# Optimization experiments

Measured on AMD Instinct MI355X. Metric: run time of the kernel, lower is better.

Reference implementation:

```python
import jax, jax.numpy as jnp
import numpy as np

T, NC, NQ = 16, 32, 32
H, W, C = 128, 128, 1
DW, DR, DZ = 256, 256, 128
LABEL_DIM, Y_DIM = 2, 2
NHEADS = 8
NFEAT = int(DW * np.log(DW))  # performer default nb_features = int(d*ln d) = 1419


def setup_inputs() -> dict:
    key = jax.random.key(0)
    ks = iter(jax.random.split(key, 48))
    def nrm(shape, scale=0.02):
        return jax.random.normal(next(ks), shape, dtype=jnp.float32) * scale
    z = lambda *s: jnp.zeros(s, jnp.float32)
    return {
        'batch_train_images': jax.random.normal(next(ks), (T, NC, C, H, W), jnp.float32),
        'label_train': jax.random.normal(next(ks), (T, NC, LABEL_DIM), jnp.float32),
        'batch_test_images': jax.random.normal(next(ks), (T, NQ, C, H, W), jnp.float32),
        'conv1_w': nrm((32, C, 3, 3), 0.1), 'conv1_b': z(32),
        'conv2_w': nrm((48, 32, 3, 3), 0.05), 'conv2_b': z(48),
        'conv3_w': nrm((64, 48, 3, 3), 0.05), 'conv3_b': z(64),
        'enc_lw': nrm((DW, 4096)), 'enc_lb': z(DW),
        'ty_w': nrm((DW // 4, LABEL_DIM)), 'ty_b': z(DW // 4),
        'er_w1': nrm((DR, DW + DW // 4), 0.05), 'er_b1': z(DR),
        'er_w2': nrm((DR, DR), 0.05), 'er_b2': z(DR),
        'er_w3': nrm((DR, DR), 0.05), 'er_b3': z(DR),
        'wq': nrm((NHEADS, DW, DW), 0.05), 'wq_b': z(NHEADS, DW),
        'wk': nrm((NHEADS, DW, DW), 0.05), 'wk_b': z(NHEADS, DW),
        'wv': nrm((NHEADS, DW, DW), 0.05), 'wv_b': z(NHEADS, DW),
        'wo_w': nrm((DW, NHEADS * DW), 0.02), 'wo_b': z(DW),
        'rz_w': nrm((DZ, DR), 0.05), 'rz_b': z(DZ),
        'd0_w1': nrm((100, DW + DZ), 0.05), 'd0_b1': z(100),
        'd0_w2': nrm((100, 100), 0.05), 'd0_b2': z(100),
        'd0_w3': nrm((Y_DIM, 100), 0.05), 'd0_b3': z(Y_DIM),
        'proj': jax.random.normal(next(ks), (NFEAT, DW), jnp.float32),
    }


def _conv(x, w, b, stride):
    y = jax.lax.conv_general_dilated(x, w, (stride, stride), [(1, 1), (1, 1)],
                                     dimension_numbers=('NCHW', 'OIHW', 'NCHW'))
    return y + b[None, :, None, None]


def _maxpool2(x):
    return jax.lax.reduce_window(x, -jnp.inf, jax.lax.max, (1, 1, 2, 2), (1, 1, 2, 2), 'VALID')


def _encode(x, c1w, c1b, c2w, c2b, c3w, c3b, lw, lb):
    # BBBEncoder (mean weights): 128->64->32->pool16->8, 64ch, flatten 4096 -> DW
    x = jax.nn.relu(_conv(x, c1w, c1b, 2))
    x = jax.nn.relu(_conv(x, c2w, c2b, 2))
    x = _maxpool2(x)
    x = jax.nn.relu(_conv(x, c3w, c3b, 2))
    x = x.reshape(x.shape[0], -1)  # [B, 4096], NCHW order matches torch view
    return x @ lw.T + lb


def _softmax_kernel(x, proj, is_query):
    # performer softmax-kernel random features
    dn = x.shape[-1] ** -0.25
    ratio = proj.shape[0] ** -0.5
    xn = x * dn
    xd = jnp.einsum('bhnd,fd->bhnf', xn, proj)
    diag = 0.5 * jnp.sum(xn * xn, axis=-1, keepdims=True)
    if is_query:
        m = jnp.max(xd, axis=-1, keepdims=True)
    else:
        m = jnp.max(xd, axis=(-1, -2), keepdims=True)
    return ratio * (jnp.exp(xd - diag - jax.lax.stop_gradient(m)) + 1e-4)


def _forward(batch_train_images, label_train, batch_test_images,
             conv1_w, conv1_b, conv2_w, conv2_b, conv3_w, conv3_b, enc_lw, enc_lb,
             ty_w, ty_b, er_w1, er_b1, er_w2, er_b2, er_w3, er_b3,
             wq, wq_b, wk, wk_b, wv, wv_b, wo_w, wo_b, rz_w, rz_b,
             d0_w1, d0_b1, d0_w2, d0_b2, d0_w3, d0_b3, proj):
    enc = lambda im: _encode(im, conv1_w, conv1_b, conv2_w, conv2_b, conv3_w, conv3_b, enc_lw, enc_lb)
    x_qry = enc(batch_test_images.reshape(-1, C, H, W)).reshape(T, NQ, DW)
    x_ctx = enc(batch_train_images.reshape(-1, C, H, W)).reshape(T, NC, DW)
    ly = label_train @ ty_w.T + ty_b
    x = jnp.concatenate([x_ctx, ly], axis=2)  # [T, NC, DW + DW//4]
    h = jax.nn.relu(x @ er_w1.T + er_b1)
    h = jax.nn.relu(h @ er_w2.T + er_b2)
    rs = h @ er_w3.T + er_b3  # [T, NC, DR]
    # per-head projections (batched over the 8 heads)
    k_all = jnp.einsum('bnd,hed->bhne', x_ctx, wk) + wk_b[None, :, None, :]
    v_all = jnp.einsum('bnd,hed->bhne', rs, wv) + wv_b[None, :, None, :]
    q_all = jnp.einsum('bnd,hed->bhne', x_qry, wq) + wq_b[None, :, None, :]
    qp = _softmax_kernel(q_all, proj, True)   # [T, H, NQ, F]
    kp = _softmax_kernel(k_all, proj, False)  # [T, H, NC, F]
    d_inv = 1.0 / jnp.einsum('bhnf,bhf->bhn', qp, kp.sum(axis=2))
    ctx_mat = jnp.einsum('bhnf,bhne->bhfe', kp, v_all)
    outs = jnp.einsum('bhnf,bhfe->bhne', qp, ctx_mat) * d_inv[..., None]
    outs = outs.transpose(0, 2, 3, 1).reshape(T, NQ, -1)  # permute(0,2,3,1).view
    rep = outs @ wo_w.T + wo_b
    zz = rep @ rz_w.T + rz_b  # [T, NQ, DZ]
    xz = jnp.concatenate([x_qry, zz], axis=-1)
    h = jax.nn.relu(xz @ d0_w1.T + d0_b1)
    h = jax.nn.relu(h @ d0_w2.T + d0_b2)
    return jnp.tanh(h @ d0_w3.T + d0_b3)  # pr_y_mu [T, NQ, Y_DIM]


def reference(batch_train_images, label_train, batch_test_images,
              conv1_w, conv1_b, conv2_w, conv2_b, conv3_w, conv3_b, enc_lw, enc_lb,
              ty_w, ty_b, er_w1, er_b1, er_w2, er_b2, er_w3, er_b3,
              wq, wq_b, wk, wk_b, wv, wv_b, wo_w, wo_b, rz_w, rz_b,
              d0_w1, d0_b1, d0_w2, d0_b2, d0_w3, d0_b3, proj):
    pr_y_mu = _forward(batch_train_images, label_train, batch_test_images,
                       conv1_w, conv1_b, conv2_w, conv2_b, conv3_w, conv3_b, enc_lw, enc_lb,
                       ty_w, ty_b, er_w1, er_b1, er_w2, er_b2, er_w3, er_b3,
                       wq, wq_b, wk, wk_b, wv, wv_b, wo_w, wo_b, rz_w, rz_b,
                       d0_w1, d0_b1, d0_w2, d0_b2, d0_w3, d0_b3, proj)
    kl = jnp.float32(0.0)  # deterministic (mean-weight) BBB encoder -> KL constant
    return (pr_y_mu, kl)
```

## Files before the change

### kernel.cpp

```cpp
#include <hip/hip_runtime.h>
#include <math.h>

#define F_FEAT 1419
static constexpr float DN    = 0.25f;

typedef short short8 __attribute__((ext_vector_type(8)));
typedef float f32x4  __attribute__((ext_vector_type(4)));

static constexpr long OFF_XDQ  = 0;
static constexpr long OFF_XDK  = 5812224;
static constexpr long U_WQH = 0;
static constexpr long U_WQL = 524288;
static constexpr long U_WKH = 1048576;
static constexpr long U_WKL = 1572864;
static constexpr long U_WVH = 2097152;
static constexpr long U_WVL = 2621440;
static constexpr long OFF_ENCT = 4000000;
static constexpr long OFF_REPT = 6200000;
static constexpr long OFF_PA   = 11624448;
static constexpr long U_PH  = 23248896;
static constexpr long U_PL  = 23625728;
static constexpr long U_XCH = 24002560;
static constexpr long U_XCL = 24264704;
static constexpr long U_RSH = 24526848;
static constexpr long U_RSL = 24657920;
static constexpr long U_C3H = 25165824;
static constexpr long U_C3L = 29360128;
static constexpr long U_WOH = 25165824;
static constexpr long U_WOL = 25690112;
static constexpr long BASE     = 16777216;
static constexpr long OFF_XCTX = BASE + 0;
static constexpr long OFF_XQRY = BASE + 131072;
static constexpr long OFF_XCAT = BASE + 262144;
static constexpr long OFF_H1   = BASE + 425984;
static constexpr long OFF_H2   = BASE + 557056;
static constexpr long OFF_RS   = BASE + 688128;
static constexpr long U_QH  = (BASE + 819200) * 2;
static constexpr long U_QL  = U_QH + 1048576;
static constexpr long U_KH  = (BASE + 1867776) * 2;
static constexpr long U_KL  = U_KH + 1048576;
static constexpr long OFF_VA   = BASE + 2916352;
static constexpr long OFF_AW1  = BASE + 3964928;
static constexpr long U_ELH = (BASE + 3977344) * 2;
static constexpr long U_ELL = U_ELH + 1048576;
static constexpr long U_REPH = U_ELH;
static constexpr long U_REPL = U_ELL;
static constexpr long OFF_REP  = BASE + 5025920;
static constexpr long OFF_XZ   = BASE + 5156992;
static constexpr long OFF_DH1  = BASE + 5353600;
static constexpr long OFF_DH2  = BASE + 5404800;
static constexpr long OFF_MD   = BASE + 5456000;
static constexpr long OFF_AW   = 22233216;
static constexpr long OFF_AW3  = 22240128;

__device__ inline unsigned short f2bf(float f) {
    unsigned int x = __float_as_uint(f);
    unsigned int r = x + 0x7fffu + ((x >> 16) & 1u);
    return (unsigned short)(r >> 16);
}
__device__ inline float bf2f(unsigned short h) {
    return __uint_as_float((unsigned int)h << 16);
}
__device__ inline unsigned int cvtpk(float a, float b) {
    unsigned int r;
    asm("v_cvt_pk_bf16_f32 %0, %1, %2" : "=v"(r) : "v"(a), "v"(b));
    return r;
}

static constexpr int NA1 = 13824;
static constexpr int NA2 = NA1 + 1024;
static constexpr int NA3 = NA2 + 73728;
static constexpr int NA4 = NA3 + 1048576;

__global__ void k_wprepA(const float* __restrict__ w2, const float* __restrict__ w1,
                         const float* __restrict__ w3, const float* __restrict__ elw,
                         unsigned short* __restrict__ Aw, unsigned short* __restrict__ Aw1,
                         unsigned short* __restrict__ Aw3,
                         unsigned short* __restrict__ ELh, unsigned short* __restrict__ ELl)
{
    int i = blockIdx.x * 256 + threadIdx.x;
    if (i < NA1) {
        int ic  = i & 31;
        int m16 = (i >> 5) & 15;
        int emt = i >> 9;
        int mt  = emt % 3, e = emt / 3;
        Aw[i] = f2bf(w2[((mt * 16 + m16) * 32 + ic) * 9 + e]);
    } else if (i < NA2) {
        int j = i - NA1;
        int k = j & 31, m = (j >> 5) & 15, mt = j >> 9;
        Aw1[j] = (k < 9) ? f2bf(w1[(mt * 16 + m) * 9 + k]) : (unsigned short)0;
    } else if (i < NA3) {
        int j = i - NA2;
        int k  = j & 63;
        int m  = (j >> 6) & 15;
        int hl = (j >> 10) & 1;
        int mt = (j >> 11) & 3;
        int e  = j >> 13;
        unsigned short v = 0;
        if (k < 48) {
            float w = w3[((mt * 16 + m) * 48 + k) * 9 + e];
            unsigned short hi = f2bf(w);
            v = hl == 0 ? hi : f2bf(w - bf2f(hi));
        }
        Aw3[j] = v;
    } else if (i < NA4) {
        int j = i - NA3;
        float v = elw[j];
        unsigned short h = f2bf(v);
        ELh[j] = h; ELl[j] = f2bf(v - bf2f(h));
    }
}

static constexpr int NB1 = 376832;
static constexpr int NB2 = NB1 + 1572864;

__global__ void k_wprepB(const float* __restrict__ proj,
                         const float* __restrict__ wq, const float* __restrict__ wk,
                         const float* __restrict__ wv,
                         unsigned short* __restrict__ Ph, unsigned short* __restrict__ Pl,
                         unsigned short* __restrict__ Wqkv)
{
    int i = blockIdx.x * 256 + threadIdx.x;
    if (i < NB1) {
        float v = (i < 363264) ? proj[i] : 0.f;
        unsigned short h = f2bf(v);
        Ph[i] = h; Pl[i] = f2bf(v - bf2f(h));
    } else if (i < NB2) {
        int j = i - NB1;
        int y = j / 524288, jj = j % 524288;
        const float* s = (y == 0) ? wq : (y == 1) ? wk : wv;
        float v = s[jj];
        unsigned short h = f2bf(v);
        Wqkv[(long)y * 1048576 + jj] = h;
        Wqkv[(long)y * 1048576 + 524288 + jj] = f2bf(v - bf2f(h));
    }
}

#define TP 136
__launch_bounds__(256)
__global__ void k_conv12m(const float* __restrict__ train, const float* __restrict__ test,
                          const float* __restrict__ b1,
                          const unsigned short* __restrict__ Aw,
                          const unsigned short* __restrict__ Aw1,
                          const float* __restrict__ b2,
                          unsigned short* __restrict__ pool_out)
{
    const int g   = blockIdx.x;
    const int img = blockIdx.y;
    const float* in = (img < 512) ? (train + (long)img * 16384)
                                  : (test  + (long)(img - 512) * 16384);

    __shared__ unsigned short ring[9 * 66 * 40];
    __shared__ unsigned short tile[19 * TP];

    const int t = threadIdx.x;

    for (int i = t; i < 9 * 40; i += 256) {
        int sl = i / 40, icp = i % 40;
        ring[(sl * 66 + 0) * 40 + icp] = 0;
    }
    if (g == 0)
        for (int i = t; i < 66 * 40; i += 256) ring[i] = 0;
    if (t < 19) *(unsigned int*)&tile[t * TP + 2] = 0u;

    {
        const float4 z4 = make_float4(0.f, 0.f, 0.f, 0.f);
        for (int u = t; u < 19 * 32; u += 256) {
            int row = u >> 5, k = u & 31;
            int r2 = 16 * g - 3 + row;
            float4 v = (r2 >= 0) ? *(const float4*)(in + r2 * 128 + k * 4) : z4;
            uint2 d;
            d.x = cvtpk(v.x, v.y);
            d.y = cvtpk(v.z, v.w);
            *(uint2*)&tile[row * TP + 4 + k * 4] = d;
        }
    }
    __syncthreads();

    const int w    = t >> 6;
    const int lane = t & 63;
    const int cn   = lane & 15;
    const int quad = lane >> 4;

    short8 a1f0 = *(const short8*)&Aw1[(0 * 16 + cn) * 32 + quad * 8];
    short8 a1f1 = *(const short8*)&Aw1[(16 + cn) * 32 + quad * 8];
    float4 bsa = *(const float4*)&b1[quad * 4];
    float4 bsb = *(const float4*)&b1[16 + quad * 4];

    const int px2 = w * 16 + cn;
    const int tb  = 2 * px2 + 2;
    auto do_slice = [&](int sl) {
        const int rb = 2 * sl * TP + tb;
        uint4 pk = make_uint4(0u, 0u, 0u, 0u);
        if (quad == 0) {
            unsigned int w00 = *(const unsigned int*)&tile[rb];
            unsigned int w10 = *(const unsigned int*)&tile[rb + 2];
            unsigned int w01 = *(const unsigned int*)&tile[rb + TP];
            unsigned int w11 = *(const unsigned int*)&tile[rb + TP + 2];
            unsigned int w02 = *(const unsigned int*)&tile[rb + 2 * TP];
            unsigned int w12 = *(const unsigned int*)&tile[rb + 2 * TP + 2];
            pk.x = (w00 >> 16) | (w10 << 16);
            pk.y = (w10 >> 16) | (w01 & 0xffff0000u);
            pk.z = w11;
            pk.w = (w02 >> 16) | (w12 << 16);
        } else if (quad == 1) {
            pk.x = (*(const unsigned int*)&tile[rb + 2 * TP + 2]) >> 16;
        }
        short8 bfr = *(const short8*)&pk;
        f32x4 z = (f32x4){0.f, 0.f, 0.f, 0.f};
        f32x4 c0 = __builtin_amdgcn_mfma_f32_16x16x32_bf16(a1f0, bfr, z, 0, 0, 0);
        f32x4 c1 = __builtin_amdgcn_mfma_f32_16x16x32_bf16(a1f1, bfr, z, 0, 0, 0);
        uint2 u0, u1;
        u0.x = cvtpk(fmaxf(c0[0] + bsa.x, 0.f), fmaxf(c0[1] + bsa.y, 0.f));
        u0.y = cvtpk(fmaxf(c0[2] + bsa.z, 0.f), fmaxf(c0[3] + bsa.w, 0.f));
        u1.x = cvtpk(fmaxf(c1[0] + bsb.x, 0.f), fmaxf(c1[1] + bsb.y, 0.f));
        u1.y = cvtpk(fmaxf(c1[2] + bsb.z, 0.f), fmaxf(c1[3] + bsb.w, 0.f));
        *(uint2*)&ring[(sl * 66 + px2 + 1) * 40 + quad * 4]      = u0;
        *(uint2*)&ring[(sl * 66 + px2 + 1) * 40 + 16 + quad * 4] = u1;
    };
    if (g > 0) do_slice(0);
    #pragma unroll
    for (int sl = 1; sl < 9; sl++) do_slice(sl);

    short8 ca0 = *(const short8*)&Aw[((0 * 3 + 0) * 16 + cn) * 32 + quad * 8];
    short8 ca1 = *(const short8*)&Aw[((0 * 3 + 1) * 16 + cn) * 32 + quad * 8];
    short8 ca2 = *(const short8*)&Aw[((0 * 3 + 2) * 16 + cn) * 32 + quad * 8];
    __syncthreads();

    const int pr = w >> 1, xh = w & 1;
    f32x4 acc[3][2];
    #pragma unroll
    for (int mt = 0; mt < 3; mt++) {
        acc[mt][0] = (f32x4){0.f, 0.f, 0.f, 0.f};
        acc[mt][1] = (f32x4){0.f, 0.f, 0.f, 0.f};
    }

    #pragma unroll
    for (int e = 0; e < 9; e++) {
        int dy = e / 3, dx = e - 3 * dy;
        int c  = 2 * (xh * 16 + cn) + dx;
        int s0 = 4 * pr + dy;
        short8 b0  = *(const short8*)&ring[(s0 * 66 + c) * 40 + quad * 8];
        short8 b1f = *(const short8*)&ring[((s0 + 2) * 66 + c) * 40 + quad * 8];
        short8 na0, na1, na2;
        if (e < 8) {
            na0 = *(const short8*)&Aw[(((e + 1) * 3 + 0) * 16 + cn) * 32 + quad * 8];
            na1 = *(const short8*)&Aw[(((e + 1) * 3 + 1) * 16 + cn) * 32 + quad * 8];
            na2 = *(const short8*)&Aw[(((e + 1) * 3 + 2) * 16 + cn) * 32 + quad * 8];
        }
        acc[0][0] = __builtin_amdgcn_mfma_f32_16x16x32_bf16(ca0, b0,  acc[0][0], 0, 0, 0);
        acc[1][0] = __builtin_amdgcn_mfma_f32_16x16x32_bf16(ca1, b0,  acc[1][0], 0, 0, 0);
        acc[2][0] = __builtin_amdgcn_mfma_f32_16x16x32_bf16(ca2, b0,  acc[2][0], 0, 0, 0);
        acc[0][1] = __builtin_amdgcn_mfma_f32_16x16x32_bf16(ca0, b1f, acc[0][1], 0, 0, 0);
        acc[1][1] = __builtin_amdgcn_mfma_f32_16x16x32_bf16(ca1, b1f, acc[1][1], 0, 0, 0);
        acc[2][1] = __builtin_amdgcn_mfma_f32_16x16x32_bf16(ca2, b1f, acc[2][1], 0, 0, 0);
        if (e < 8) { ca0 = na0; ca1 = na1; ca2 = na2; }
    }

    {
        const int prow = 2 * g + pr;
        const int ppx  = xh * 8 + (cn >> 1);
        unsigned short* pb = pool_out + ((long)img * 256 + prow * 16 + ppx) * 96
                           + ((cn & 1) ? 48 : 0);
        #pragma unroll
        for (int mt = 0; mt < 3; mt++) {
            float4 bv = *(const float4*)&b2[mt * 16 + quad * 4];
            float m0, m1, m2, m3;
            {
                float v;
                v = fmaxf(fmaxf(acc[mt][0][0] + bv.x, acc[mt][1][0] + bv.x), 0.f);
                m0 = fmaxf(v, __shfl_xor(v, 1));
                v = fmaxf(fmaxf(acc[mt][0][1] + bv.y, acc[mt][1][1] + bv.y), 0.f);
                m1 = fmaxf(v, __shfl_xor(v, 1));
                v = fmaxf(fmaxf(acc[mt][0][2] + bv.z, acc[mt][1][2] + bv.z), 0.f);
                m2 = fmaxf(v, __shfl_xor(v, 1));
                v = fmaxf(fmaxf(acc[mt][0][3] + bv.w, acc[mt][1][3] + bv.w), 0.f);
                m3 = fmaxf(v, __shfl_xor(v, 1));
            }
            uint2 hv;
            hv.x = cvtpk(m0, m1);
            hv.y = cvtpk(m2, m3);
            uint2 sv = hv;
            if (cn & 1) {
                float d0 = m0 - bf2f((unsigned short)(hv.x & 0xffffu));
                float d1 = m1 - bf2f((unsigned short)(hv.x >> 16));
                float d2 = m2 - bf2f((unsigned short)(hv.y & 0xffffu));
                float d3 = m3 - bf2f((unsigned short)(hv.y >> 16));
                sv.x = cvtpk(d0, d1);
                sv.y = cvtpk(d2, d3);
            }
            *(uint2*)&pb[mt * 16 + quad * 4] = sv;
        }
    }
}

#define C3PITCH 104
__launch_bounds__(512)
__global__ void k_conv3m(const unsigned short* __restrict__ pool,
                         const unsigned short* __restrict__ Aw3,
                         const float* __restrict__ b3,
                         unsigned short* __restrict__ C3h, unsigned short* __restrict__ C3l)
{
    const int img = blockIdx.x;
    __shared__ unsigned short s_in[30120];
    const int t = threadIdx.x;

    uint4* s4 = (uint4*)s_in;
    const uint4 zz = make_uint4(0, 0, 0, 0);
    for (int i = t; i < 3765; i += 512) s4[i] = zz;
    __syncthreads();
    {
        int p = t >> 1, half = t & 1;
        const uint4* src = (const uint4*)(pool + ((long)img * 256 + p) * 96 + half * 48);
        int r = p >> 4, c = p & 15;
        uint4* dst = (uint4*)(s_in + ((r + 1) * 17 + (c + 1)) * C3PITCH + half * 48);
        #pragma unroll
        for (int j = 0; j < 6; j++) dst[j] = src[j];
    }
    __syncthreads();

    const int w = t >> 6, lane = t & 63;
    const int n = lane & 15, quad = lane >> 4;
    const int mt = w >> 1, ntb = (w & 1) * 2;

    f32x4 acc[2];
    acc[0] = (f32x4){0.f, 0.f, 0.f, 0.f};
    acc[1] = (f32x4){0.f, 0.f, 0.f, 0.f};

    for (int e = 0; e < 9; e++) {
        int dy = e / 3, dx = e - 3 * dy;
        const unsigned short* A0 = Aw3 + (long)(((e * 4 + mt) * 2 + 0) * 16 + n) * 64 + quad * 8;
        const unsigned short* A1 = Aw3 + (long)(((e * 4 + mt) * 2 + 1) * 16 + n) * 64 + quad * 8;
        short8 ah0 = *(const short8*)(A0);
        short8 ah1 = *(const short8*)(A0 + 32);
        short8 al0 = *(const short8*)(A1);
        short8 al1 = *(const short8*)(A1 + 32);
        #pragma unroll
        for (int j = 0; j < 2; j++) {
            int p = (ntb + j) * 16 + n;
            int y = p >> 3, x = p & 7;
            const unsigned short* Bp = s_in + ((2 * y + dy) * 17 + (2 * x + dx)) * C3PITCH + quad * 8;
            short8 bh0 = *(const short8*)(Bp);
            short8 bh1 = *(const short8*)(Bp + 32);
            short8 bl0 = *(const short8*)(Bp + 48);
            short8 bl1 = *(const short8*)(Bp + 48 + 32);
            acc[j] = __builtin_amdgcn_mfma_f32_16x16x32_bf16(ah0, bh0, acc[j], 0, 0, 0);
            acc[j] = __builtin_amdgcn_mfma_f32_16x16x32_bf16(ah1, bh1, acc[j], 0, 0, 0);
            acc[j] = __builtin_amdgcn_mfma_f32_16x16x32_bf16(ah0, bl0, acc[j], 0, 0, 0);
            acc[j] = __builtin_amdgcn_mfma_f32_16x16x32_bf16(ah1, bl1, acc[j], 0, 0, 0);
            acc[j] = __builtin_amdgcn_mfma_f32_16x16x32_bf16(al0, bh0, acc[j], 0, 0, 0);
            acc[j] = __builtin_amdgcn_mfma_f32_16x16x32_bf16(al1, bh1, acc[j], 0, 0, 0);
        }
    }

    unsigned short* oh = C3h + (long)img * 4096;
    unsigned short* ol = C3l + (long)img * 4096;
    #pragma unroll
    for (int reg = 0; reg < 4; reg++) {
        int oc = mt * 16 + quad * 4 + reg;
        float bias = b3[oc];
        #pragma unroll
        for (int j = 0; j < 2; j++) {
            int p = (ntb + j) * 16 + n;
            float v = fmaxf(acc[j][reg] + bias, 0.f);
            unsigned short h = f2bf(v);
            oh[oc * 64 + p] = h;
            ol[oc * 64 + p] = f2bf(v - bf2f(h));
        }
    }
}

template<int OUTMODE>
__launch_bounds__(256)
__global__ void mgemm(const unsigned short* __restrict__ Xh0, const unsigned short* __restrict__ Xl0,
                      const unsigned short* __restrict__ Wph, const unsigned short* __restrict__ Wpl,
                      const float* __restrict__ Bb, float* __restrict__ Yf,
                      unsigned short* __restrict__ Yh, unsigned short* __restrict__ Yl,
                      int M, int N, int K, int ldY, float scale,
                      long sX, long sW, long sB, long sY, int kChunk)
{
    const int z = blockIdx.z;
    const unsigned short* Xh = Xh0 + (OUTMODE == 3 ? 0 : (long)z * sX);
    const unsigned short* Xl = Xl0 + (OUTMODE == 3 ? 0 : (long)z * sX);
    const unsigned short* Wh = Wph + (OUTMODE == 3 ? 0 : (long)z * sW);
    const unsigned short* Wl = Wpl + (OUTMODE == 3 ? 0 : (long)z * sW);
    const float* B = Bb ? (Bb + (OUTMODE == 3 ? 0 : (long)z * sB)) : nullptr;
    int k0 = 0, k1 = K;
    if (OUTMODE == 3) { k0 = z * kChunk; k1 = min(K, k0 + kChunk); }

    __shared__ unsigned short sAh[64 * 40], sAl[64 * 40], sBh[64 * 40], sBl[64 * 40];

    const int t = threadIdx.x;
    const int m0 = blockIdx.y * 64, n0 = blockIdx.x * 64;
    const int r = t >> 2, kq = (t & 3) * 8;

    const int w = t >> 6, lane = t & 63;
    const int wm = (w & 1) * 32, wn = (w >> 1) * 32;
    const int cn = lane & 15, quad = lane >> 4;

    f32x4 acc[2][2];
    acc[0][0] = acc[0][1] = acc[1][0] = acc[1][1] = (f32x4){0.f, 0.f, 0.f, 0.f};

    for (int kb = k0; kb < k1; kb += 32) {
        *(uint4*)&sAh[r * 40 + kq] = *(const uint4*)&Xh[(long)(m0 + r) * K + kb + kq];
        *(uint4*)&sAl[r * 40 + kq] = *(const uint4*)&Xl[(long)(m0 + r) * K + kb + kq];
        *(uint4*)&sBh[r * 40 + kq] = *(const uint4*)&Wh[(long)(n0 + r) * K + kb + kq];
        *(uint4*)&sBl[r * 40 + kq] = *(const uint4*)&Wl[(long)(n0 + r) * K + kb + kq];
        __syncthreads();
        short8 axh[2], axl[2], bxh[2], bxl[2];
        #pragma unroll
        for (int i = 0; i < 2; i++) {
            axh[i] = *(const short8*)&sAh[(wm + i * 16 + cn) * 40 + quad * 8];
            axl[i] = *(const short8*)&sAl[(wm + i * 16 + cn) * 40 + quad * 8];
            bxh[i] = *(const short8*)&sBh[(wn + i * 16 + cn) * 40 + quad * 8];
            bxl[i] = *(const short8*)&sBl[(wn + i * 16 + cn) * 40 + quad * 8];
        }
        #pragma unroll
        for (int i = 0; i < 2; i++)
            #pragma unroll
            for (int j = 0; j < 2; j++) {
                acc[i][j] = __builtin_amdgcn_mfma_f32_16x16x32_bf16(axh[i], bxh[j], acc[i][j], 0, 0, 0);
                acc[i][j] = __builtin_amdgcn_mfma_f32_16x16x32_bf16(axh[i], bxl[j], acc[i][j], 0, 0, 0);
                acc[i][j] = __builtin_amdgcn_mfma_f32_16x16x32_bf16(axl[i], bxh[j], acc[i][j], 0, 0, 0);
            }
        __syncthreads();
    }

    #pragma unroll
    for (int i = 0; i < 2; i++) {
        #pragma unroll
        for (int reg = 0; reg < 4; reg++) {
            int row = m0 + wm + i * 16 + quad * 4 + reg;
            #pragma unroll
            for (int j = 0; j < 2; j++) {
                int col = n0 + wn + j * 16 + cn;
                if (col >= N) continue;
                float v = acc[i][j][reg] * scale;
                if (OUTMODE == 3) {
                    (Yf + (long)z * sY)[(long)row * ldY + col] = v;
                } else if (OUTMODE == 0) {
                    if (B) v += B[col];
                    (Yf + (long)z * sY)[(long)row * ldY + col] = v;
                } else {
                    if (B) v += B[col];
                    unsigned short h = f2bf(v);
                    (Yh + (long)z * sY)[(long)row * ldY + col] = h;
                    (Yl + (long)z * sY)[(long)row * ldY + col] = f2bf(v - bf2f(h));
                }
            }
        }
    }
}

__global__ void k_red_enc(const float* __restrict__ tmp, const float* __restrict__ elb,
                          float* __restrict__ x_ctx, unsigned short* __restrict__ XCh,
                          unsigned short* __restrict__ XCl, float* __restrict__ xcat,
                          const float* __restrict__ label, const float* __restrict__ tyw,
                          const float* __restrict__ tyb,
                          const float* __restrict__ wow, unsigned short* __restrict__ WOh,
                          unsigned short* __restrict__ WOl)
{
    int b = blockIdx.x;
    int tt = threadIdx.x;
    if (b < 1024) {
        int i = b * 256 + tt;
        int r = i >> 8, c = i & 255;
        float v = elb[c];
        #pragma unroll
        for (int z = 0; z < 8; z++) v += tmp[(long)z * 262144 + i];
        x_ctx[i] = v;
        unsigned short h = f2bf(v);
        XCh[i] = h; XCl[i] = f2bf(v - bf2f(h));
        if (r < 512) xcat[r * 320 + c] = v;
    } else if (b < 1152) {
        int i = (b - 1024) * 256 + tt;
        int r = i >> 6, e = i & 63;
        xcat[r * 320 + 256 + e] = tyb[e] + label[r * 2] * tyw[e * 2] + label[r * 2 + 1] * tyw[e * 2 + 1];
    } else {
        int i = (b - 1152) * 256 + tt;
        float v = wow[i];
        unsigned short h = f2bf(v);
        WOh[i] = h; WOl[i] = f2bf(v - bf2f(h));
    }
}

__global__ void k_red_rep(const float* __restrict__ tmp, const float* __restrict__ wob,
                          float* __restrict__ rep,
                          const float* __restrict__ xq, float* __restrict__ xz)
{
    int b = blockIdx.x;
    int tt = threadIdx.x;
    if (b < 512) {
        int i = b * 256 + tt;
        int c = i & 255;
        float v = wob[c];
        #pragma unroll
        for (int z = 0; z < 4; z++) v += tmp[(long)z * 131072 + i];
        rep[i] = v;
    } else {
        int i = (b - 512) * 256 + tt;
        int r = i >> 8, c = i & 255;
        xz[r * 384 + c] = xq[i];
    }
}

template<int BM, int BN, int BK, int ACT, bool FIN, bool WP>
__launch_bounds__(256)
__global__ void gemm_k(const float* __restrict__ X, const float* __restrict__ W,
                       const float* __restrict__ B, float* __restrict__ Y,
                       int M, int N, int K, int ldY,
                       unsigned short* __restrict__ Ph2, unsigned short* __restrict__ Pl2)
{
    __shared__ float As[BK][BM + 4];
    __shared__ float Bs[BK][BN + 4];
    const int t = threadIdx.x;
    const int tx = t & 15, ty = t >> 4;
    const int m0 = blockIdx.y * BM, n0 = blockIdx.x * BN;
    float acc[2][2] = {{0.f, 0.f}, {0.f, 0.f}};

    for (int kb = 0; kb < K; kb += BK) {
        for (int i = t; i < BM * BK; i += 256) {
            int rr = i / BK, c = i % BK;
            int mm = m0 + rr, kk = kb + c;
            As[c][rr] = (mm < M && kk < K) ? X[(long)mm * K + kk] : 0.f;
        }
        for (int i = t; i < BN * BK; i += 256) {
            int rr = i / BK, c = i % BK;
            int nn = n0 + rr, kk = kb + c;
            Bs[c][rr] = (nn < N && kk < K) ? W[(long)nn * K + kk] : 0.f;
        }
        __syncthreads();
        #pragma unroll
        for (int kk = 0; kk < BK; kk++) {
            float2 a2 = *(const float2*)&As[kk][ty * 2];
            float2 b2 = *(const float2*)&Bs[kk][tx * 2];
            acc[0][0] += a2.x * b2.x; acc[0][1] += a2.x * b2.y;
            acc[1][0] += a2.y * b2.x; acc[1][1] += a2.y * b2.y;
        }
        __syncthreads();
    }

    #pragma unroll
    for (int i = 0; i < 2; i++) {
        int mm = m0 + ty * 2 + i;
        if (mm >= M) continue;
        #pragma unroll
        for (int j = 0; j < 2; j++) {
            int nn = n0 + tx * 2 + j;
            if (nn >= N) continue;
            float v = acc[i][j] + (B ? B[nn] : 0.f);
            if (ACT == 1) v = fmaxf(v, 0.f);
            if (ACT == 2) v = tanhf(v);
            Y[(long)mm * ldY + nn] = v;
            if (WP) {
                unsigned short h = f2bf(v);
                Ph2[(long)mm * ldY + nn] = h;
                Pl2[(long)mm * ldY + nn] = f2bf(v - bf2f(h));
            }
        }
    }
    if (FIN && t == 0 && blockIdx.x == 0 && blockIdx.y == 0) Y[1024] = 0.f;
}

__launch_bounds__(256)
__global__ void k_maxdiag(const float* __restrict__ xdq, const float* __restrict__ xdk,
                          const unsigned short* __restrict__ Qh, const unsigned short* __restrict__ Ql,
                          const unsigned short* __restrict__ Kh, const unsigned short* __restrict__ Kl,
                          float* __restrict__ dq, float* __restrict__ mq,
                          float* __restrict__ dk, float* __restrict__ mk)
{
    __shared__ float red[8];
    const int bx = blockIdx.x;
    const int t = threadIdx.x;

    if (bx < 4096) {
        const int tok = bx;
        float v = bf2f(Qh[(long)tok * 256 + t]) + bf2f(Ql[(long)tok * 256 + t]);
        float s = v * v;
        for (int d = 1; d < 64; d <<= 1) s += __shfl_xor(s, d);
        if ((t & 63) == 0) red[t >> 6] = s;

        float m = -1e30f;
        #pragma unroll
        for (int j = 0; j < 6; j++) {
            int f = t + j * 256;
            if (f < F_FEAT) m = fmaxf(m, xdq[(long)tok * F_FEAT + f]);
        }
        for (int d = 1; d < 64; d <<= 1) m = fmaxf(m, __shfl_xor(m, d));
        if ((t & 63) == 0) red[4 + (t >> 6)] = m;
        __syncthreads();
        if (t == 0) {
            dq[tok] = (red[0] + red[1] + red[2] + red[3]) * (1.f / 32.f);
            mq[tok] = fmaxf(fmaxf(red[4], red[5]), fmaxf(red[6], red[7]));
        }
    } else {
        const int kb = bx - 4096;
        const long tok0 = (long)kb * 32;
        const int row = t >> 3, j = t & 7;

        float s = 0.f;
        const unsigned short* ph = Kh + (tok0 + row) * 256 + j * 32;
        const unsigned short* pl = Kl + (tok0 + row) * 256 + j * 32;
        for (int q = 0; q < 32; q++) { float v = bf2f(ph[q]) + bf2f(pl[q]); s += v * v; }
        s += __shfl_xor(s, 1); s += __shfl_xor(s, 2); s += __shfl_xor(s, 4);
        if (j == 0) dk[tok0 + row] = s * (1.f / 32.f);

        const float* base = xdk + tok0 * F_FEAT;
        float m = -1e30f;
        for (int i = t; i < 32 * F_FEAT; i += 256) m = fmaxf(m, base[i]);
        for (int d = 1; d < 64; d <<= 1) m = fmaxf(m, __shfl_xor(m, d));
        if ((t & 63) == 0) red[t >> 6] = m;
        __syncthreads();
        if (t == 0) mk[kb] = fmaxf(fmaxf(red[0], red[1]), fmaxf(red[2], red[3]));
    }
}

#define NSPLIT 4
#define FCH 355
__launch_bounds__(256)
__global__ void k_attn1(const float* __restrict__ qp, const float* __restrict__ kp,
                        const float* __restrict__ dq, const float* __restrict__ mq,
                        const float* __restrict__ dk, const float* __restrict__ mk,
                        float* __restrict__ pA)
{
    const int s  = blockIdx.x;
    const int kb = blockIdx.y;
    const long row0 = (long)kb * 32;
    const int f0 = s * FCH;
    const int f1 = min(F_FEAT, f0 + FCH);

    __shared__ float s_q[32 * 65];
    __shared__ float s_k[32 * 65];
    __shared__ float s_cq[32], s_ck[32];

    const int t = threadIdx.x;
    const int n = t >> 3;
    const int mq_ = (t & 7) * 4;

    if (t < 32) {
        s_cq[t] = dq[row0 + t] + mq[row0 + t];
        s_ck[t] = dk[row0 + t] + mk[kb];
    }
    __syncthreads();

    float acc[4] = {0.f, 0.f, 0.f, 0.f};
    for (int fc = f0; fc < f1; fc += 64) {
        for (int i = t; i < 2048; i += 256) {
            int rr = i >> 6, ff = i & 63;
            int fg = fc + ff;
            float qv = 0.f, kv = 0.f;
            if (fg < f1) {
                qv = expf(qp[(row0 + rr) * F_FEAT + fg] - s_cq[rr]) + 1e-4f;
                kv = expf(kp[(row0 + rr) * F_FEAT + fg] - s_ck[rr]) + 1e-4f;
            }
            s_q[rr * 65 + ff] = qv;
            s_k[rr * 65 + ff] = kv;
        }
        __syncthreads();
        #pragma unroll 8
        for (int ff = 0; ff < 64; ff++) {
            float a = s_q[n * 65 + ff];
            #pragma unroll
            for (int j = 0; j < 4; j++) acc[j] += a * s_k[(mq_ + j) * 65 + ff];
        }
        __syncthreads();
    }

    float* dst = pA + ((long)kb * NSPLIT + s) * 1024;
    #pragma unroll
    for (int j = 0; j < 4; j++) dst[n * 32 + mq_ + j] = acc[j];
}

__launch_bounds__(256)
__global__ void k_attn2(const float* __restrict__ pA, const float* __restrict__ va,
                        unsigned short* __restrict__ REPh, unsigned short* __restrict__ REPl)
{
    const int ec = blockIdx.x;
    const int kb = blockIdx.y;
    const int h = kb >> 4, tt = kb & 15;
    const long row0 = (long)kb * 32;

    __shared__ float s_A[32][33];
    __shared__ float s_di[32];
    __shared__ float s_v[32 * 64];

    const int t = threadIdx.x;

    {
        const float* base = pA + (long)kb * NSPLIT * 1024 + t * 4;
        float4 v0 = *(const float4*)(base);
        float4 v1 = *(const float4*)(base + 1024);
        float4 v2 = *(const float4*)(base + 2048);
        float4 v3 = *(const float4*)(base + 3072);
        int r = t >> 3, c = (t & 7) * 4;
        s_A[r][c]     = v0.x + v1.x + v2.x + v3.x;
        s_A[r][c + 1] = v0.y + v1.y + v2.y + v3.y;
        s_A[r][c + 2] = v0.z + v1.z + v2.z + v3.z;
        s_A[r][c + 3] = v0.w + v1.w + v2.w + v3.w;
    }
    for (int i = t; i < 2048; i += 256) {
        int m = i >> 6, e = i & 63;
        s_v[m * 64 + e] = va[row0 * 256 + m * 256 + ec * 64 + e];
    }
    __syncthreads();
    if (t < 32) {
        float s = 0.f;
        #pragma unroll
        for (int m = 0; m < 32; m++) s += s_A[t][m];
        s_di[t] = 1.f / s;
    }
    __syncthreads();

    const int n = t >> 3, e0 = t & 7;
    float out[8];
    #pragma unroll
    for (int j = 0; j < 8; j++) out[j] = 0.f;
    for (int m = 0; m < 32; m++) {
        float a = s_A[n][m];
        #pragma unroll
        for (int j = 0; j < 8; j++) out[j] += a * s_v[m * 64 + e0 + 8 * j];
    }
    float di = s_di[n];
    unsigned short* dsth = REPh + ((long)tt * 32 + n) * 2048;
    unsigned short* dstl = REPl + ((long)tt * 32 + n) * 2048;
    #pragma unroll
    for (int j = 0; j < 8; j++) {
        int e = ec * 64 + e0 + 8 * j;
        float val = out[j] * di;
        unsigned short hh = f2bf(val);
        dsth[e * 8 + h] = hh;
        dstl[e * 8 + h] = f2bf(val - bf2f(hh));
    }
}

extern "C" void kernel_launch(void* const* d_in, const int* in_sizes, int n_in,
                              void* d_out, int out_size, void* d_ws, size_t ws_size,
                              hipStream_t stream)
{
    const float* train  = (const float*)d_in[0];
    const float* label  = (const float*)d_in[1];
    const float* test   = (const float*)d_in[2];
    const float* c1w = (const float*)d_in[3];  const float* c1b = (const float*)d_in[4];
    const float* c2w = (const float*)d_in[5];  const float* c2b = (const float*)d_in[6];
    const float* c3w = (const float*)d_in[7];  const float* c3b = (const float*)d_in[8];
    const float* elw = (const float*)d_in[9];  const float* elb = (const float*)d_in[10];
    const float* tyw = (const float*)d_in[11]; const float* tyb = (const float*)d_in[12];
    const float* ew1 = (const float*)d_in[13]; const float* eb1 = (const float*)d_in[14];
    const float* ew2 = (const float*)d_in[15]; const float* eb2 = (const float*)d_in[16];
    const float* ew3 = (const float*)d_in[17]; const float* eb3 = (const float*)d_in[18];
    const float* wq  = (const float*)d_in[19]; const float* wqb = (const float*)d_in[20];
    const float* wk  = (const float*)d_in[21]; const float* wkb = (const float*)d_in[22];
    const float* wv  = (const float*)d_in[23]; const float* wvb = (const float*)d_in[24];
    const float* wow = (const float*)d_in[25]; const float* wob = (const float*)d_in[26];
    const float* rzw = (const float*)d_in[27]; const float* rzb = (const float*)d_in[28];
    const float* dw1 = (const float*)d_in[29]; const float* db1 = (const float*)d_in[30];
    const float* dw2 = (const float*)d_in[31]; const float* db2 = (const float*)d_in[32];
    const float* dw3 = (const float*)d_in[33]; const float* db3 = (const float*)d_in[34];
    const float* proj= (const float*)d_in[35];

    float* wsf = (float*)d_ws;
    unsigned short* usw = (unsigned short*)d_ws;
    float* out = (float*)d_out;

    unsigned short* A_pool = usw;
    float* x_ctx  = wsf + OFF_XCTX;
    float* x_qry  = wsf + OFF_XQRY;
    float* xcat   = wsf + OFF_XCAT;
    float* h1     = wsf + OFF_H1;
    float* h2     = wsf + OFF_H2;
    float* rs     = wsf + OFF_RS;
    float* v_all  = wsf + OFF_VA;
    float* rep    = wsf + OFF_REP;
    float* xz     = wsf + OFF_XZ;
    float* dh1    = wsf + OFF_DH1;
    float* dh2    = wsf + OFF_DH2;
    float* xd_q   = wsf + OFF_XDQ;
    float* xd_k   = wsf + OFF_XDK;
    float* enc_t  = wsf + OFF_ENCT;
    float* rep_t  = wsf + OFF_REPT;
    float* pA     = wsf + OFF_PA;
    float* dqv    = wsf + OFF_MD;
    float* mqv    = wsf + OFF_MD + 4096;
    float* dkv    = wsf + OFF_MD + 8192;
    float* mkv    = wsf + OFF_MD + 12288;
    unsigned short* Aw  = (unsigned short*)(wsf + OFF_AW);
    unsigned short* Aw3 = (unsigned short*)(wsf + OFF_AW3);
    unsigned short* Aw1 = (unsigned short*)(wsf + OFF_AW1);

    unsigned short* Wqkv = usw + U_WQH;
    unsigned short* WQh = usw + U_WQH; unsigned short* WQl = usw + U_WQL;
    unsigned short* WKh = usw + U_WKH; unsigned short* WKl = usw + U_WKL;
    unsigned short* WVh = usw + U_WVH; unsigned short* WVl = usw + U_WVL;
    unsigned short* Ph  = usw + U_PH;  unsigned short* Pl  = usw + U_PL;
    unsigned short* XCh = usw + U_XCH; unsigned short* XCl = usw + U_XCL;
    unsigned short* RSh = usw + U_RSH; unsigned short* RSl = usw + U_RSL;
    unsigned short* C3h = usw + U_C3H; unsigned short* C3l = usw + U_C3L;
    unsigned short* Qh  = usw + U_QH;  unsigned short* Ql  = usw + U_QL;
    unsigned short* Kh  = usw + U_KH;  unsigned short* Kl  = usw + U_KL;
    unsigned short* ELh = usw + U_ELH; unsigned short* ELl = usw + U_ELL;
    unsigned short* WOh = usw + U_WOH; unsigned short* WOl = usw + U_WOL;
    unsigned short* REPh= usw + U_REPH;unsigned short* REPl= usw + U_REPL;

    k_wprepA<<<4442, 256, 0, stream>>>(c2w, c1w, c3w, elw, Aw, Aw1, Aw3, ELh, ELl);

    k_conv12m<<<dim3(8, 1024), 256, 0, stream>>>(train, test, c1b, Aw, Aw1, c2b, A_pool);
    k_conv3m<<<1024, 512, 0, stream>>>(A_pool, Aw3, c3b, C3h, C3l);

    k_wprepB<<<7616, 256, 0, stream>>>(proj, wq, wk, wv, Ph, Pl, Wqkv);

    mgemm<3><<<dim3(4, 16, 8), 256, 0, stream>>>(
        C3h, C3l, ELh, ELl, nullptr, enc_t, nullptr, nullptr,
        1024, 256, 4096, 256, 1.f, 0, 0, 0, 262144, 512);
    k_red_enc<<<3200, 256, 0, stream>>>(enc_t, elb, x_ctx, XCh, XCl, xcat,
                                        label, tyw, tyb, wow, WOh, WOl);

    gemm_k<32,32,32,1,false,false><<<dim3(8, 16), 256, 0, stream>>>(xcat, ew1, eb1, h1, 512, 256, 320, 256, nullptr, nullptr);
    gemm_k<32,32,32,1,false,false><<<dim3(8, 16), 256, 0, stream>>>(h1, ew2, eb2, h2, 512, 256, 256, 256, nullptr, nullptr);
    gemm_k<32,32,32,0,false,true ><<<dim3(8, 16), 256, 0, stream>>>(h2, ew3, eb3, rs, 512, 256, 256, 256, RSh, RSl);

    mgemm<1><<<dim3(4, 8, 8), 256, 0, stream>>>(
        XCh + 512 * 256, XCl + 512 * 256, WQh, WQl, wqb, nullptr, Qh, Ql,
        512, 256, 256, 256, 1.f, 0, 65536, 256, 131072, 0);
    mgemm<1><<<dim3(4, 8, 8), 256, 0, stream>>>(
        XCh, XCl, WKh, WKl, wkb, nullptr, Kh, Kl,
        512, 256, 256, 256, 1.f, 0, 65536, 256, 131072, 0);
    mgemm<0><<<dim3(4, 8, 8), 256, 0, stream>>>(
        RSh, RSl, WVh, WVl, wvb, v_all, nullptr, nullptr,
        512, 256, 256, 256, 1.f, 0, 65536, 256, 131072, 0);

    mgemm<0><<<dim3(23, 64, 2), 256, 0, stream>>>(
        Qh, Ql, Ph, Pl, nullptr, xd_q, nullptr, nullptr,
        4096, F_FEAT, 256, F_FEAT, DN, 2097152, 0, 0, 5812224, 0);

    k_maxdiag<<<4224, 256, 0, stream>>>(xd_q, xd_k, Qh, Ql, Kh, Kl, dqv, mqv, dkv, mkv);

    k_attn1<<<dim3(NSPLIT, 128), 256, 0, stream>>>(xd_q, xd_k, dqv, mqv, dkv, mkv, pA);
    k_attn2<<<dim3(4, 128), 256, 0, stream>>>(pA, v_all, REPh, REPl);

    mgemm<3><<<dim3(4, 8, 4), 256, 0, stream>>>(
        REPh, REPl, WOh, WOl, nullptr, rep_t, nullptr, nullptr,
        512, 256, 2048, 256, 1.f, 0, 0, 0, 131072, 512);
    k_red_rep<<<1024, 256, 0, stream>>>(rep_t, wob, rep, x_qry, xz);

    gemm_k<32,32,32,0,false,false><<<dim3(4, 16), 256, 0, stream>>>(rep, rzw, rzb, xz + 256, 512, 128, 256, 384, nullptr, nullptr);

    gemm_k<32,32,32,1,false,false><<<dim3(4, 16), 256, 0, stream>>>(xz, dw1, db1, dh1, 512, 100, 384, 100, nullptr, nullptr);
    gemm_k<32,32,32,1,false,false><<<dim3(4, 16), 256, 0, stream>>>(dh1, dw2, db2, dh2, 512, 100, 100, 100, nullptr, nullptr);
    gemm_k<32,32,32,2,true ,false><<<dim3(1, 16), 256, 0, stream>>>(dh2, dw3, db3, out, 512, 2, 100, 2, nullptr, nullptr);
}
```

Baseline: 698.1 us.

## Fuse QKV GEMMs and fold max/diag reductions into GEMM epilogues

```diff
diff --git a/kernel.cpp b/kernel.cpp
--- a/kernel.cpp
+++ b/kernel.cpp
@@ -66,6 +66,13 @@
     asm("v_cvt_pk_bf16_f32 %0, %1, %2" : "=v"(r) : "v"(a), "v"(b));
     return r;
 }
+__device__ inline unsigned encf(float f) {
+    unsigned u = __float_as_uint(f);
+    return (u & 0x80000000u) ? ~u : (u | 0x80000000u);
+}
+__device__ inline float decf(unsigned u) {
+    return __uint_as_float((u & 0x80000000u) ? (u & 0x7fffffffu) : ~u);
+}
 
 static constexpr int NA1 = 13824;
 static constexpr int NA2 = NA1 + 1024;
@@ -377,7 +384,8 @@
                       const float* __restrict__ Bb, float* __restrict__ Yf,
                       unsigned short* __restrict__ Yh, unsigned short* __restrict__ Yl,
                       int M, int N, int K, int ldY, float scale,
-                      long sX, long sW, long sB, long sY, int kChunk)
+                      long sX, long sW, long sB, long sY, int kChunk,
+                      unsigned* __restrict__ mqe, unsigned* __restrict__ mke)
 {
     const int z = blockIdx.z;
     const unsigned short* Xh = Xh0 + (OUTMODE == 3 ? 0 : (long)z * sX);
@@ -426,11 +434,13 @@
         __syncthreads();
     }
 
+    float gmax = -3e38f;
     #pragma unroll
     for (int i = 0; i < 2; i++) {
         #pragma unroll
         for (int reg = 0; reg < 4; reg++) {
             int row = m0 + wm + i * 16 + quad * 4 + reg;
+            float rmax = -3e38f;
             #pragma unroll
             for (int j = 0; j < 2; j++) {
                 int col = n0 + wn + j * 16 + cn;
@@ -438,9 +448,10 @@
                 float v = acc[i][j][reg] * scale;
                 if (OUTMODE == 3) {
                     (Yf + (long)z * sY)[(long)row * ldY + col] = v;
-                } else if (OUTMODE == 0) {
+                } else if (OUTMODE == 0 || OUTMODE == 5) {
                     if (B) v += B[col];
                     (Yf + (long)z * sY)[(long)row * ldY + col] = v;
+                    if (OUTMODE == 5) rmax = fmaxf(rmax, v);
                 } else {
                     if (B) v += B[col];
                     unsigned short h = f2bf(v);
@@ -448,6 +459,108 @@
                     (Yl + (long)z * sY)[(long)row * ldY + col] = f2bf(v - bf2f(h));
                 }
             }
+            if (OUTMODE == 5) {
+                if (z == 0) {
+                    rmax = fmaxf(rmax, __shfl_xor(rmax, 1));
+                    rmax = fmaxf(rmax, __shfl_xor(rmax, 2));
+                    rmax = fmaxf(rmax, __shfl_xor(rmax, 4));
+                    rmax = fmaxf(rmax, __shfl_xor(rmax, 8));
+                    if (cn == 0) atomicMax(&mqe[row], encf(rmax));
+                } else {
+                    gmax = fmaxf(gmax, rmax);
+                }
+            }
+        }
+    }
+    if (OUTMODE == 5 && z == 1) {
+        for (int d = 1; d < 64; d <<= 1) gmax = fmaxf(gmax, __shfl_xor(gmax, d));
+        if (lane == 0) atomicMax(&mke[(m0 + wm) >> 5], encf(gmax));
+    }
+}
+
+__launch_bounds__(256)
+__global__ void k_qkv(const unsigned short* __restrict__ XCh, const unsigned short* __restrict__ XCl,
+                      const unsigned short* __restrict__ RSh, const unsigned short* __restrict__ RSl,
+                      const unsigned short* __restrict__ Wqkv,
+                      const float* __restrict__ wqb, const float* __restrict__ wkb,
+                      const float* __restrict__ wvb,
+                      unsigned short* __restrict__ Qh, unsigned short* __restrict__ Ql,
+                      unsigned short* __restrict__ Kh, unsigned short* __restrict__ Kl,
+                      float* __restrict__ v_all, float* __restrict__ dq, float* __restrict__ dk)
+{
+    const int z = blockIdx.z, y = z >> 3, zh = z & 7;
+    const unsigned short* Xh = (y == 0) ? XCh + 512 * 256 : (y == 1) ? XCh : RSh;
+    const unsigned short* Xl = (y == 0) ? XCl + 512 * 256 : (y == 1) ? XCl : RSl;
+    const unsigned short* Wh = Wqkv + (long)y * 1048576 + (long)zh * 65536;
+    const unsigned short* Wl = Wh + 524288;
+    const float* B = ((y == 0) ? wqb : (y == 1) ? wkb : wvb) + zh * 256;
+
+    __shared__ unsigned short sAh[64 * 40], sAl[64 * 40], sBh[64 * 40], sBl[64 * 40];
+
+    const int t = threadIdx.x;
+    const int m0 = blockIdx.y * 64, n0 = blockIdx.x * 64;
+    const int r = t >> 2, kq = (t & 3) * 8;
+    const int w = t >> 6, lane = t & 63;
+    const int wm = (w & 1) * 32, wn = (w >> 1) * 32;
+    const int cn = lane & 15, quad = lane >> 4;
+
+    f32x4 acc[2][2];
+    acc[0][0] = acc[0][1] = acc[1][0] = acc[1][1] = (f32x4){0.f, 0.f, 0.f, 0.f};
+
+    for (int kb = 0; kb < 256; kb += 32) {
+        *(uint4*)&sAh[r * 40 + kq] = *(const uint4*)&Xh[(long)(m0 + r) * 256 + kb + kq];
+        *(uint4*)&sAl[r * 40 + kq] = *(const uint4*)&Xl[(long)(m0 + r) * 256 + kb + kq];
+        *(uint4*)&sBh[r * 40 + kq] = *(const uint4*)&Wh[(long)(n0 + r) * 256 + kb + kq];
+        *(uint4*)&sBl[r * 40 + kq] = *(const uint4*)&Wl[(long)(n0 + r) * 256 + kb + kq];
+        __syncthreads();
+        short8 axh[2], axl[2], bxh[2], bxl[2];
+        #pragma unroll
+        for (int i = 0; i < 2; i++) {
+            axh[i] = *(const short8*)&sAh[(wm + i * 16 + cn) * 40 + quad * 8];
+            axl[i] = *(const short8*)&sAl[(wm + i * 16 + cn) * 40 + quad * 8];
+            bxh[i] = *(const short8*)&sBh[(wn + i * 16 + cn) * 40 + quad * 8];
+            bxl[i] = *(const short8*)&sBl[(wn + i * 16 + cn) * 40 + quad * 8];
+        }
+        #pragma unroll
+        for (int i = 0; i < 2; i++)
+            #pragma unroll
+            for (int j = 0; j < 2; j++) {
+                acc[i][j] = __builtin_amdgcn_mfma_f32_16x16x32_bf16(axh[i], bxh[j], acc[i][j], 0, 0, 0);
+                acc[i][j] = __builtin_amdgcn_mfma_f32_16x16x32_bf16(axh[i], bxl[j], acc[i][j], 0, 0, 0);
+                acc[i][j] = __builtin_amdgcn_mfma_f32_16x16x32_bf16(axl[i], bxh[j], acc[i][j], 0, 0, 0);
+            }
+        __syncthreads();
+    }
+
+    unsigned short* Yh = ((y == 0) ? Qh : Kh) + (long)zh * 131072;
+    unsigned short* Yl = ((y == 0) ? Ql : Kl) + (long)zh * 131072;
+    float* Yf = v_all + (long)zh * 131072;
+    float* dacc = ((y == 0) ? dq : dk) + zh * 512;
+
+    #pragma unroll
+    for (int i = 0; i < 2; i++) {
+        #pragma unroll
+        for (int reg = 0; reg < 4; reg++) {
+            int row = m0 + wm + i * 16 + quad * 4 + reg;
+            float s = 0.f;
+            #pragma unroll
+            for (int j = 0; j < 2; j++) {
+                int col = n0 + wn + j * 16 + cn;
+                float v = acc[i][j][reg] + B[col];
+                if (y == 2) {
+                    Yf[(long)row * 256 + col] = v;
+                } else {
+                    unsigned short h = f2bf(v);
+                    Yh[(long)row * 256 + col] = h;
+                    Yl[(long)row * 256 + col] = f2bf(v - bf2f(h));
+                    s += v * v;
+                }
+            }
+            if (y < 2) {
+                s += __shfl_xor(s, 1); s += __shfl_xor(s, 2);
+                s += __shfl_xor(s, 4); s += __shfl_xor(s, 8);
+                if (cn == 0) atomicAdd(&dacc[row], s * (1.f / 32.f));
+            }
         }
     }
 }
@@ -458,7 +571,7 @@
                           const float* __restrict__ label, const float* __restrict__ tyw,
                           const float* __restrict__ tyb,
                           const float* __restrict__ wow, unsigned short* __restrict__ WOh,
-                          unsigned short* __restrict__ WOl)
+                          unsigned short* __restrict__ WOl, unsigned* __restrict__ md)
 {
     int b = blockIdx.x;
     int tt = threadIdx.x;
@@ -476,11 +589,14 @@
         int i = (b - 1024) * 256 + tt;
         int r = i >> 6, e = i & 63;
         xcat[r * 320 + 256 + e] = tyb[e] + label[r * 2] * tyw[e * 2] + label[r * 2 + 1] * tyw[e * 2 + 1];
-    } else {
+    } else if (b < 3200) {
         int i = (b - 1152) * 256 + tt;
         float v = wow[i];
         unsigned short h = f2bf(v);
         WOh[i] = h; WOl[i] = f2bf(v - bf2f(h));
+    } else {
+        int i = (b - 3200) * 256 + tt;
+        if (i < 12416) md[i] = 0u;
     }
 }
 
@@ -495,7 +611,7 @@
         int c = i & 255;
         float v = wob[c];
         #pragma unroll
-        for (int z = 0; z < 4; z++) v += tmp[(long)z * 131072 + i];
+        for (int z = 0; z < 8; z++) v += tmp[(long)z * 131072 + i];
         rep[i] = v;
     } else {
         int i = (b - 512) * 256 + tt;
@@ -562,65 +678,12 @@
     if (FIN && t == 0 && blockIdx.x == 0 && blockIdx.y == 0) Y[1024] = 0.f;
 }
 
-__launch_bounds__(256)
-__global__ void k_maxdiag(const float* __restrict__ xdq, const float* __restrict__ xdk,
-                          const unsigned short* __restrict__ Qh, const unsigned short* __restrict__ Ql,
-                          const unsigned short* __restrict__ Kh, const unsigned short* __restrict__ Kl,
-                          float* __restrict__ dq, float* __restrict__ mq,
-                          float* __restrict__ dk, float* __restrict__ mk)
-{
-    __shared__ float red[8];
-    const int bx = blockIdx.x;
-    const int t = threadIdx.x;
-
-    if (bx < 4096) {
-        const int tok = bx;
-        float v = bf2f(Qh[(long)tok * 256 + t]) + bf2f(Ql[(long)tok * 256 + t]);
-        float s = v * v;
-        for (int d = 1; d < 64; d <<= 1) s += __shfl_xor(s, d);
-        if ((t & 63) == 0) red[t >> 6] = s;
-
-        float m = -1e30f;
-        #pragma unroll
-        for (int j = 0; j < 6; j++) {
-            int f = t + j * 256;
-            if (f < F_FEAT) m = fmaxf(m, xdq[(long)tok * F_FEAT + f]);
-        }
-        for (int d = 1; d < 64; d <<= 1) m = fmaxf(m, __shfl_xor(m, d));
-        if ((t & 63) == 0) red[4 + (t >> 6)] = m;
-        __syncthreads();
-        if (t == 0) {
-            dq[tok] = (red[0] + red[1] + red[2] + red[3]) * (1.f / 32.f);
-            mq[tok] = fmaxf(fmaxf(red[4], red[5]), fmaxf(red[6], red[7]));
-        }
-    } else {
-        const int kb = bx - 4096;
-        const long tok0 = (long)kb * 32;
-        const int row = t >> 3, j = t & 7;
-
-        float s = 0.f;
-        const unsigned short* ph = Kh + (tok0 + row) * 256 + j * 32;
-        const unsigned short* pl = Kl + (tok0 + row) * 256 + j * 32;
-        for (int q = 0; q < 32; q++) { float v = bf2f(ph[q]) + bf2f(pl[q]); s += v * v; }
-        s += __shfl_xor(s, 1); s += __shfl_xor(s, 2); s += __shfl_xor(s, 4);
-        if (j == 0) dk[tok0 + row] = s * (1.f / 32.f);
-
-        const float* base = xdk + tok0 * F_FEAT;
-        float m = -1e30f;
-        for (int i = t; i < 32 * F_FEAT; i += 256) m = fmaxf(m, base[i]);
-        for (int d = 1; d < 64; d <<= 1) m = fmaxf(m, __shfl_xor(m, d));
-        if ((t & 63) == 0) red[t >> 6] = m;
-        __syncthreads();
-        if (t == 0) mk[kb] = fmaxf(fmaxf(red[0], red[1]), fmaxf(red[2], red[3]));
-    }
-}
-
 #define NSPLIT 4
 #define FCH 355
 __launch_bounds__(256)
 __global__ void k_attn1(const float* __restrict__ qp, const float* __restrict__ kp,
-                        const float* __restrict__ dq, const float* __restrict__ mq,
-                        const float* __restrict__ dk, const float* __restrict__ mk,
+                        const float* __restrict__ dq, const unsigned* __restrict__ mqe,
+                        const float* __restrict__ dk, const unsigned* __restrict__ mke,
                         float* __restrict__ pA)
 {
     const int s  = blockIdx.x;
@@ -638,8 +701,8 @@
     const int mq_ = (t & 7) * 4;
 
     if (t < 32) {
-        s_cq[t] = dq[row0 + t] + mq[row0 + t];
-        s_ck[t] = dk[row0 + t] + mk[kb];
+        s_cq[t] = dq[row0 + t] + decf(mqe[row0 + t]);
+        s_ck[t] = dk[row0 + t] + decf(mke[kb]);
     }
     __syncthreads();
 
@@ -650,8 +713,8 @@
             int fg = fc + ff;
             float qv = 0.f, kv = 0.f;
             if (fg < f1) {
-                qv = expf(qp[(row0 + rr) * F_FEAT + fg] - s_cq[rr]) + 1e-4f;
-                kv = expf(kp[(row0 + rr) * F_FEAT + fg] - s_ck[rr]) + 1e-4f;
+                qv = __expf(qp[(row0 + rr) * F_FEAT + fg] - s_cq[rr]) + 1e-4f;
+                kv = __expf(kp[(row0 + rr) * F_FEAT + fg] - s_ck[rr]) + 1e-4f;
             }
             s_q[rr * 65 + ff] = qv;
             s_k[rr * 65 + ff] = kv;
@@ -780,17 +843,15 @@
     float* rep_t  = wsf + OFF_REPT;
     float* pA     = wsf + OFF_PA;
     float* dqv    = wsf + OFF_MD;
-    float* mqv    = wsf + OFF_MD + 4096;
+    unsigned* mqe = (unsigned*)(wsf + OFF_MD + 4096);
     float* dkv    = wsf + OFF_MD + 8192;
-    float* mkv    = wsf + OFF_MD + 12288;
+    unsigned* mke = (unsigned*)(wsf + OFF_MD + 12288);
+    unsigned* mdw = (unsigned*)(wsf + OFF_MD);
     unsigned short* Aw  = (unsigned short*)(wsf + OFF_AW);
     unsigned short* Aw3 = (unsigned short*)(wsf + OFF_AW3);
     unsigned short* Aw1 = (unsigned short*)(wsf + OFF_AW1);
 
     unsigned short* Wqkv = usw + U_WQH;
-    unsigned short* WQh = usw + U_WQH; unsigned short* WQl = usw + U_WQL;
-    unsigned short* WKh = usw + U_WKH; unsigned short* WKl = usw + U_WKL;
-    unsigned short* WVh = usw + U_WVH; unsigned short* WVl = usw + U_WVL;
     unsigned short* Ph  = usw + U_PH;  unsigned short* Pl  = usw + U_PL;
     unsigned short* XCh = usw + U_XCH; unsigned short* XCl = usw + U_XCL;
     unsigned short* RSh = usw + U_RSH; unsigned short* RSl = usw + U_RSL;
@@ -810,36 +871,28 @@
 
     mgemm<3><<<dim3(4, 16, 8), 256, 0, stream>>>(
         C3h, C3l, ELh, ELl, nullptr, enc_t, nullptr, nullptr,
-        1024, 256, 4096, 256, 1.f, 0, 0, 0, 262144, 512);
-    k_red_enc<<<3200, 256, 0, stream>>>(enc_t, elb, x_ctx, XCh, XCl, xcat,
-                                        label, tyw, tyb, wow, WOh, WOl);
+        1024, 256, 4096, 256, 1.f, 0, 0, 0, 262144, 512, nullptr, nullptr);
+    k_red_enc<<<3249, 256, 0, stream>>>(enc_t, elb, x_ctx, XCh, XCl, xcat,
+                                        label, tyw, tyb, wow, WOh, WOl, mdw);
 
     gemm_k<32,32,32,1,false,false><<<dim3(8, 16), 256, 0, stream>>>(xcat, ew1, eb1, h1, 512, 256, 320, 256, nullptr, nullptr);
     gemm_k<32,32,32,1,false,false><<<dim3(8, 16), 256, 0, stream>>>(h1, ew2, eb2, h2, 512, 256, 256, 256, nullptr, nullptr);
     gemm_k<32,32,32,0,false,true ><<<dim3(8, 16), 256, 0, stream>>>(h2, ew3, eb3, rs, 512, 256, 256, 256, RSh, RSl);
 
-    mgemm<1><<<dim3(4, 8, 8), 256, 0, stream>>>(
-        XCh + 512 * 256, XCl + 512 * 256, WQh, WQl, wqb, nullptr, Qh, Ql,
-        512, 256, 256, 256, 1.f, 0, 65536, 256, 131072, 0);
-    mgemm<1><<<dim3(4, 8, 8), 256, 0, stream>>>(
-        XCh, XCl, WKh, WKl, wkb, nullptr, Kh, Kl,
-        512, 256, 256, 256, 1.f, 0, 65536, 256, 131072, 0);
-    mgemm<0><<<dim3(4, 8, 8), 256, 0, stream>>>(
-        RSh, RSl, WVh, WVl, wvb, v_all, nullptr, nullptr,
-        512, 256, 256, 256, 1.f, 0, 65536, 256, 131072, 0);
-
-    mgemm<0><<<dim3(23, 64, 2), 256, 0, stream>>>(
+    k_qkv<<<dim3(4, 8, 24), 256, 0, stream>>>(XCh, XCl, RSh, RSl, Wqkv,
+                                              wqb, wkb, wvb, Qh, Ql, Kh, Kl,
+                                              v_all, dqv, dkv);
+
+    mgemm<5><<<dim3(23, 64, 2), 256, 0, stream>>>(
         Qh, Ql, Ph, Pl, nullptr, xd_q, nullptr, nullptr,
-        4096, F_FEAT, 256, F_FEAT, DN, 2097152, 0, 0, 5812224, 0);
-
-    k_maxdiag<<<4224, 256, 0, stream>>>(xd_q, xd_k, Qh, Ql, Kh, Kl, dqv, mqv, dkv, mkv);
-
-    k_attn1<<<dim3(NSPLIT, 128), 256, 0, stream>>>(xd_q, xd_k, dqv, mqv, dkv, mkv, pA);
+        4096, F_FEAT, 256, F_FEAT, DN, 2097152, 0, 0, 5812224, 0, mqe, mke);
+
+    k_attn1<<<dim3(NSPLIT, 128), 256, 0, stream>>>(xd_q, xd_k, dqv, mqe, dkv, mke, pA);
     k_attn2<<<dim3(4, 128), 256, 0, stream>>>(pA, v_all, REPh, REPl);
 
-    mgemm<3><<<dim3(4, 8, 4), 256, 0, stream>>>(
+    mgemm<3><<<dim3(4, 8, 8), 256, 0, stream>>>(
         REPh, REPl, WOh, WOl, nullptr, rep_t, nullptr, nullptr,
-        512, 256, 2048, 256, 1.f, 0, 0, 0, 131072, 512);
+        512, 256, 2048, 256, 1.f, 0, 0, 0, 131072, 256, nullptr, nullptr);
     k_red_rep<<<1024, 256, 0, stream>>>(rep_t, wob, rep, x_qry, xz);
 
     gemm_k<32,32,32,0,false,false><<<dim3(4, 16), 256, 0, stream>>>(rep, rzw, rzb, xz + 256, 512, 128, 256, 384, nullptr, nullptr);
```

After: 650.1 us, median of 2. 1.07x faster.
